# Kernel tuning notes

Measured on AMD Instinct MI355X. Metric: run time of the kernel, lower is better.

## Reference

```python
import jax, jax.numpy as jnp
import numpy as np

H = 8        # num_heads
LN_EPS = 1e-5
NEG = -1000000.0


def setup_inputs() -> dict:
    key = jax.random.key(0)
    ks = jax.random.split(key, 8)
    B, T, D = 4, 4096, 1024
    s = 1.0 / np.sqrt(D)
    x = jax.random.normal(ks[0], (B, T, D), dtype=jnp.float32)
    tmask = (jnp.arange(T) < (3 * T) // 4).astype(jnp.float32)
    src_mask = jnp.broadcast_to(tmask[None, :, None], (B, T, 1)).astype(jnp.float32)
    Wq = jax.random.normal(ks[1], (D, D), dtype=jnp.float32) * s
    Wk = jax.random.normal(ks[2], (D, D), dtype=jnp.float32) * s
    Wv = jax.random.normal(ks[3], (D, D), dtype=jnp.float32) * s
    bq = jnp.zeros((D,), jnp.float32)
    bk = jnp.zeros((D,), jnp.float32)
    bv = jnp.zeros((D,), jnp.float32)
    gamma = jnp.ones((D,), jnp.float32)
    beta = jnp.zeros((D,), jnp.float32)
    return {"x": x, "src_mask": src_mask, "Wq": Wq, "bq": bq, "Wk": Wk,
            "bk": bk, "Wv": Wv, "bv": bv, "gamma": gamma, "beta": beta}


def reference(x, src_mask, Wq, bq, Wk, bk, Wv, bv, gamma, beta):
    B, T, D = x.shape
    Dh = D // H
    # LayerNorm (same normed input feeds q, k, v)
    mu = jnp.mean(x, axis=-1, keepdims=True)
    var = jnp.mean(jnp.square(x - mu), axis=-1, keepdims=True)
    xn = (x - mu) * jax.lax.rsqrt(var + LN_EPS) * gamma + beta
    q = xn @ Wq + bq                               # [B,T,D]
    k = xn @ Wk + bk + (1.0 - src_mask) * NEG      # mask padded timesteps
    v = (xn @ Wv + bv) * src_mask                  # zero padded values
    q = jax.nn.softmax(q.reshape(B, T, H, Dh), axis=-1)   # over feature dim
    k = jax.nn.softmax(k.reshape(B, T, H, Dh), axis=1)    # over time dim
    v = v.reshape(B, T, H, Dh)
    # efficient/linear attention: O(T * Dh^2) per head
    att = jnp.einsum('bnhd,bnhl->bhdl', k, v)      # [B,H,Dh,Dh]
    y = jnp.einsum('bnhd,bhdl->bnhl', q, att).reshape(B, T, D)
    return x + y
```

## Files before the change

### kernel.cpp

```cpp
#include <hip/hip_runtime.h>
#include <stdint.h>


typedef unsigned short u16;
typedef __attribute__((ext_vector_type(8))) short bf16x8;
typedef __attribute__((ext_vector_type(4))) float f32x4;

__device__ u16 g_WT[3][1024 * 1024];
__device__ u16 g_xn[16777216];
__device__ u16 g_ekT[16777216];
__device__ u16 g_vvT[16777216];
__device__ float g_attp[8388608];
__device__ u16 g_attT[524288];
__device__ float g_Z[4096];

__device__ __forceinline__ float b2f(u16 u) {
  union { unsigned int i; float f; } c;
  c.i = ((unsigned int)u) << 16;
  return c.f;
}
__device__ __forceinline__ u16 f2b(float f) {
  union { float f; unsigned int i; } c;
  c.f = f;
  unsigned int r = c.i + 0x7fffu + ((c.i >> 16) & 1u);
  return (u16)(r >> 16);
}

__device__ __forceinline__ void gload16(const void* g, void* l) {
  __builtin_amdgcn_global_load_lds(
      reinterpret_cast<const __attribute__((address_space(1))) uint32_t*>(
          reinterpret_cast<uintptr_t>(g)),
      reinterpret_cast<__attribute__((address_space(3))) uint32_t*>(
          reinterpret_cast<uintptr_t>(l)),
      16, 0, 0);
}

__device__ __forceinline__ void stage128x32(const u16* g, int stride, char* lds,
                                            int wave, int lane) {
  const int r = wave * 32 + (lane >> 2);
  const int cb = (lane & 3) * 16;
  const char* gp = (const char*)g;
  gload16(gp + (size_t)r * stride * 2 + cb, lds + wave * 2048);
  gload16(gp + (size_t)(r + 16) * stride * 2 + cb, lds + wave * 2048 + 1024);
}

__device__ __forceinline__ bf16x8 frag_ld(const char* lds, int row, int lane) {
  return *(const bf16x8*)(lds + row * 64 + ((lane >> 4) * 16));
}

__device__ __forceinline__ void tile_mfma(const char* As, const char* Bs,
                                          f32x4 (&acc)[4][4], int wm, int wn,
                                          int lane) {
  bf16x8 af[4], bfr[4];
#pragma unroll
  for (int i = 0; i < 4; i++) af[i] = frag_ld(As, wm * 64 + i * 16 + (lane & 15), lane);
#pragma unroll
  for (int j = 0; j < 4; j++) bfr[j] = frag_ld(Bs, wn * 64 + j * 16 + (lane & 15), lane);
#pragma unroll
  for (int i = 0; i < 4; i++)
#pragma unroll
    for (int j = 0; j < 4; j++)
      acc[i][j] = __builtin_amdgcn_mfma_f32_16x16x32_bf16(af[i], bfr[j], acc[i][j], 0, 0, 0);
}

__device__ __forceinline__ void stageA256(char* buf, const u16* gsrc, int h,
                                          int wave, int lane) {
#pragma unroll
  for (int i = 0; i < 2; i++) {
    const int ib = i * 64 + wave * 8;
    const int rowb = (ib & 63) | ((ib & 64) << 1) | (h << 6);
    const int row = rowb + (lane >> 3);
    const int cc = (lane & 7) ^ (row & 7);
    gload16((const char*)gsrc + ((size_t)row * 1024 + cc * 8) * 2,
            buf + rowb * 128);
  }
}
__device__ __forceinline__ void stageB256(char* buf, const u16* gsrc, int h,
                                          int wave, int lane) {
#pragma unroll
  for (int i = 0; i < 2; i++) {
    const int ib = i * 64 + wave * 8;
    const int rowb = (ib & 31) | ((ib & 96) << 1) | (h << 5);
    const int row = rowb + (lane >> 3);
    const int cc = (lane & 7) ^ (row & 7);
    gload16((const char*)gsrc + ((size_t)row * 1024 + cc * 8) * 2,
            buf + rowb * 128);
  }
}
__device__ __forceinline__ bf16x8 fragS(const char* buf, int R, int ks, int lane) {
  const int q = lane >> 4;
  return *(const bf16x8*)(buf + R * 128 + ((((ks << 2) + q) ^ (R & 7)) << 4));
}

__global__ __launch_bounds__(256) void prep_kernel(const float* __restrict__ x,
                                                   const float* __restrict__ gamma,
                                                   const float* __restrict__ beta,
                                                   const float* __restrict__ wq,
                                                   const float* __restrict__ wk,
                                                   const float* __restrict__ wv) {
  __shared__ float ls[4], ls2[4];
  __shared__ u16 tile[32][33];
  const int bid = blockIdx.x;
  const int tid = threadIdx.x;
  if (bid < 16384) {
    if (bid < 16) g_Z[bid * 256 + tid] = 0.0f;
    const int wave = tid >> 6, lane = tid & 63;
    const float* xr = x + (size_t)bid * 1024;
    float4 u = ((const float4*)xr)[tid];
    float v0 = u.x, v1 = u.y, v2 = u.z, v3 = u.w;
    float s = v0 + v1 + v2 + v3;
    float s2 = v0 * v0 + v1 * v1 + v2 * v2 + v3 * v3;
#pragma unroll
    for (int off = 32; off > 0; off >>= 1) {
      s += __shfl_down(s, off);
      s2 += __shfl_down(s2, off);
    }
    if (lane == 0) { ls[wave] = s; ls2[wave] = s2; }
    __syncthreads();
    s = ls[0] + ls[1] + ls[2] + ls[3];
    s2 = ls2[0] + ls2[1] + ls2[2] + ls2[3];
    const float mu = s * (1.0f / 1024.0f);
    const float var = fmaxf(s2 * (1.0f / 1024.0f) - mu * mu, 0.0f);
    const float rstd = rsqrtf(var + 1e-5f);
    float4 g4 = ((const float4*)gamma)[tid];
    float4 be = ((const float4*)beta)[tid];
    ushort4 o;
    o.x = f2b((v0 - mu) * rstd * g4.x + be.x);
    o.y = f2b((v1 - mu) * rstd * g4.y + be.y);
    o.z = f2b((v2 - mu) * rstd * g4.z + be.z);
    o.w = f2b((v3 - mu) * rstd * g4.w + be.w);
    *(ushort4*)(g_xn + (size_t)bid * 1024 + tid * 4) = o;
  } else {
    const int id = bid - 16384;
    const int which = id >> 10;
    const int rem = id & 1023;
    const float* src = (which == 0) ? wq : (which == 1) ? wk : wv;
    u16* dst = g_WT[which];
    const int tx = tid & 31;
    const int ty = tid >> 5;
    const int c0 = (rem & 31) * 32, r0 = (rem >> 5) * 32;
#pragma unroll
    for (int i = 0; i < 4; i++)
      tile[ty + i * 8][tx] = f2b(src[(size_t)(r0 + ty + i * 8) * 1024 + c0 + tx]);
    __syncthreads();
#pragma unroll
    for (int i = 0; i < 4; i++)
      dst[(size_t)(c0 + ty + i * 8) * 1024 + r0 + tx] = tile[tx][ty + i * 8];
  }
}

__global__ __launch_bounds__(512, 2) void gemm_kv(const float* __restrict__ bk,
                                                  const float* __restrict__ bv,
                                                  const float* __restrict__ mask) {
  __shared__ __align__(16) char smem[131072];
  const int tid = threadIdx.x, wave = tid >> 6, lane = tid & 63;
  const int L = blockIdx.x;
  const int mt = (L & 7) + 8 * (L >> 6);
  const int nt = (L >> 3) & 7;
  const int n0 = (nt & 3) * 256;
  const int z = nt >> 2;
  const int m0 = mt * 256;
  const u16* wt = z ? g_WT[2] : g_WT[1];
  const float* bias = z ? bv : bk;
  u16* outT = z ? g_vvT : g_ekT;
  const int b = m0 >> 12;
  const int t0 = m0 & 4095;
  const int wm = wave >> 2, wn = wave & 3;
  const u16* Ag = g_xn + (size_t)m0 * 1024;
  const u16* Bg = wt + (size_t)n0 * 1024;

  f32x4 zero = {0.f, 0.f, 0.f, 0.f};
  f32x4 acc[8][4];
#pragma unroll
  for (int i = 0; i < 8; i++)
#pragma unroll
    for (int j = 0; j < 4; j++) acc[i][j] = zero;
  bf16x8 a[4][2], bB[2][2][2];

  stageA256(smem, Ag, 0, wave, lane);
  stageB256(smem + 65536, Bg, 0, wave, lane);
  stageA256(smem, Ag, 1, wave, lane);
  stageB256(smem + 65536, Bg, 1, wave, lane);
  asm volatile("s_waitcnt vmcnt(0)" ::: "memory");
  __builtin_amdgcn_s_barrier();

#pragma unroll 1
  for (int t = 0; t < 16; ++t) {
    const int p = t & 1;
    char* Ab = smem + p * 32768;
    char* Bb = smem + 65536 + p * 32768;
    char* An = smem + (p ^ 1) * 32768;
    char* Bn = smem + 65536 + (p ^ 1) * 32768;
    const u16* Agn = Ag + (t + 1) * 64;
    const u16* Bgn = Bg + (t + 1) * 64;
    const bool st = t < 15;

#pragma unroll
    for (int rf = 0; rf < 4; rf++) {
      const int R = wm * 128 + rf * 16 + (lane & 15);
#pragma unroll
      for (int ks = 0; ks < 2; ks++) a[rf][ks] = fragS(Ab, R, ks, lane);
    }
#pragma unroll
    for (int cf = 0; cf < 2; cf++) {
      const int R = wn * 64 + cf * 16 + (lane & 15);
#pragma unroll
      for (int ks = 0; ks < 2; ks++) bB[0][cf][ks] = fragS(Bb, R, ks, lane);
    }
    if (st) {
      stageA256(An, Agn, 0, wave, lane);
      stageB256(Bn, Bgn, 0, wave, lane);
      asm volatile("s_waitcnt vmcnt(4)" ::: "memory");
    } else {
      asm volatile("s_waitcnt vmcnt(0)" ::: "memory");
    }
    __builtin_amdgcn_s_barrier();
    asm volatile("s_waitcnt lgkmcnt(0)" ::: "memory");
    __builtin_amdgcn_sched_barrier(0);
    __builtin_amdgcn_s_setprio(1);
#pragma unroll
    for (int rf = 0; rf < 4; rf++)
#pragma unroll
      for (int cf = 0; cf < 2; cf++)
#pragma unroll
        for (int ks = 0; ks < 2; ks++)
          acc[rf][cf] = __builtin_amdgcn_mfma_f32_16x16x32_bf16(
              a[rf][ks], bB[0][cf][ks], acc[rf][cf], 0, 0, 0);
    __builtin_amdgcn_s_setprio(0);
    __builtin_amdgcn_s_barrier();
    __builtin_amdgcn_sched_barrier(0);

#pragma unroll
    for (int cf = 0; cf < 2; cf++) {
      const int R = wn * 64 + 32 + cf * 16 + (lane & 15);
#pragma unroll
      for (int ks = 0; ks < 2; ks++) bB[1][cf][ks] = fragS(Bb, R, ks, lane);
    }
    if (st) stageB256(Bn, Bgn, 1, wave, lane);
    __builtin_amdgcn_s_barrier();
    asm volatile("s_waitcnt lgkmcnt(0)" ::: "memory");
    __builtin_amdgcn_sched_barrier(0);
    __builtin_amdgcn_s_setprio(1);
#pragma unroll
    for (int rf = 0; rf < 4; rf++)
#pragma unroll
      for (int cf = 0; cf < 2; cf++)
#pragma unroll
        for (int ks = 0; ks < 2; ks++)
          acc[rf][2 + cf] = __builtin_amdgcn_mfma_f32_16x16x32_bf16(
              a[rf][ks], bB[1][cf][ks], acc[rf][2 + cf], 0, 0, 0);
    __builtin_amdgcn_s_setprio(0);
    __builtin_amdgcn_s_barrier();
    __builtin_amdgcn_sched_barrier(0);

#pragma unroll
    for (int rf = 0; rf < 4; rf++) {
      const int R = wm * 128 + 64 + rf * 16 + (lane & 15);
#pragma unroll
      for (int ks = 0; ks < 2; ks++) a[rf][ks] = fragS(Ab, R, ks, lane);
    }
    if (st) stageA256(An, Agn, 1, wave, lane);
    asm volatile("s_waitcnt vmcnt(4)" ::: "memory");
    __builtin_amdgcn_s_barrier();
    asm volatile("s_waitcnt lgkmcnt(0)" ::: "memory");
    __builtin_amdgcn_sched_barrier(0);
    __builtin_amdgcn_s_setprio(1);
#pragma unroll
    for (int rf = 0; rf < 4; rf++)
#pragma unroll
      for (int cf = 0; cf < 2; cf++)
#pragma unroll
        for (int ks = 0; ks < 2; ks++)
          acc[4 + rf][2 + cf] = __builtin_amdgcn_mfma_f32_16x16x32_bf16(
              a[rf][ks], bB[1][cf][ks], acc[4 + rf][2 + cf], 0, 0, 0);
    __builtin_amdgcn_s_setprio(0);
    __builtin_amdgcn_s_barrier();
    __builtin_amdgcn_sched_barrier(0);

    asm volatile("s_waitcnt vmcnt(2)" ::: "memory");
    __builtin_amdgcn_s_barrier();
    __builtin_amdgcn_s_setprio(1);
#pragma unroll
    for (int rf = 0; rf < 4; rf++)
#pragma unroll
      for (int cf = 0; cf < 2; cf++)
#pragma unroll
        for (int ks = 0; ks < 2; ks++)
          acc[4 + rf][cf] = __builtin_amdgcn_mfma_f32_16x16x32_bf16(
              a[rf][ks], bB[0][cf][ks], acc[4 + rf][cf], 0, 0, 0);
    __builtin_amdgcn_s_setprio(0);
    __builtin_amdgcn_s_barrier();
    __builtin_amdgcn_sched_barrier(0);
  }

  u16* tT = (u16*)smem;
  float fsum[4] = {0.f, 0.f, 0.f, 0.f};
#pragma unroll
  for (int rf = 0; rf < 8; rf++)
#pragma unroll
    for (int r = 0; r < 4; r++) {
      const int tok = wm * 128 + rf * 16 + (lane >> 4) * 4 + r;
      const float mv = mask[m0 + tok];
#pragma unroll
      for (int cf = 0; cf < 4; cf++) {
        const int feat = wn * 64 + cf * 16 + (lane & 15);
        const float aV = acc[rf][cf][r] + bias[n0 + feat];
        float o;
        if (z)
          o = aV * mv;
        else
          o = (mv > 0.5f) ? __expf(fminf(aV, 30.0f)) : 0.0f;
        const u16 ob = f2b(o);
        tT[feat * 256 + ((((tok >> 3) ^ (feat & 7)) << 3) | (tok & 7))] = ob;
        if (!z) fsum[cf] += b2f(ob);
      }
    }
  if (!z) {
#pragma unroll
    for (int cf = 0; cf < 4; cf++) {
      float s = fsum[cf];
      s += __shfl_xor(s, 16);
      s += __shfl_xor(s, 32);
      if (lane < 16)
        atomicAdd(&g_Z[b * 1024 + n0 + wn * 64 + cf * 16 + lane], s);
    }
  }
  __syncthreads();
  const size_t gbase = (size_t)b * (1024 * 4096) + (size_t)n0 * 4096 + t0;
#pragma unroll
  for (int u = 0; u < 16; u++) {
    const int id = u * 512 + tid;
    const int feat = id >> 5, c = id & 31;
    uint4 val = *(const uint4*)&tT[feat * 256 + ((c ^ (feat & 7)) << 3)];
    *(uint4*)(outT + gbase + (size_t)feat * 4096 + c * 8) = val;
  }
}

__global__ __launch_bounds__(256) void gemm_att() {
  __shared__ __align__(16) char smem[32768];
  char* A0 = smem;
  char* B0 = smem + 8192;
  char* A1 = smem + 16384;
  char* B1 = smem + 24576;
  const int tid = threadIdx.x, wave = tid >> 6, lane = tid & 63;
  const int kc = blockIdx.x;
  const int bh = blockIdx.y;
  const int b = bh >> 3, h = bh & 7;
  const size_t base = (size_t)b * (1024 * 4096) + (size_t)(h * 128) * 4096;
  const int wm = wave & 1, wn = wave >> 1;
  const u16* Ag = g_ekT + base + kc * 256;
  const u16* Bg = g_vvT + base + kc * 256;

  f32x4 zero = {0.f, 0.f, 0.f, 0.f};
  f32x4 acc[4][4];
#pragma unroll
  for (int i = 0; i < 4; i++)
#pragma unroll
    for (int j = 0; j < 4; j++) acc[i][j] = zero;

  stage128x32(Ag, 4096, A0, wave, lane);
  stage128x32(Bg, 4096, B0, wave, lane);
  __syncthreads();
  for (int kt = 0; kt < 256; kt += 64) {
    stage128x32(Ag + kt + 32, 4096, A1, wave, lane);
    stage128x32(Bg + kt + 32, 4096, B1, wave, lane);
    tile_mfma(A0, B0, acc, wm, wn, lane);
    __syncthreads();
    if (kt + 64 < 256) {
      stage128x32(Ag + kt + 64, 4096, A0, wave, lane);
      stage128x32(Bg + kt + 64, 4096, B0, wave, lane);
    }
    tile_mfma(A1, B1, acc, wm, wn, lane);
    __syncthreads();
  }

  float* op = g_attp + ((size_t)(kc * 32 + bh)) * 16384;
#pragma unroll
  for (int i = 0; i < 4; i++)
#pragma unroll
    for (int r = 0; r < 4; r++) {
      const int row = wm * 64 + i * 16 + (lane >> 4) * 4 + r;
#pragma unroll
      for (int j = 0; j < 4; j++) {
        const int col = wn * 64 + j * 16 + (lane & 15);
        op[row * 128 + col] = acc[i][j][r];
      }
    }
}

__global__ __launch_bounds__(256) void attnorm_kernel() {
  const int bh = blockIdx.x;
  const int b = bh >> 3, h = bh & 7;
  const int tid = threadIdx.x;
  __shared__ float Zl[128];
  if (tid < 128) Zl[tid] = fmaxf(g_Z[b * 1024 + h * 128 + tid], 1e-30f);
  __syncthreads();
  const int i0 = blockIdx.y * 2048;
  for (int i = i0 + tid; i < i0 + 2048; i += 256) {
    const int d = i >> 7, l = i & 127;
    float s = 0.f;
#pragma unroll
    for (int c = 0; c < 16; c++) s += g_attp[((size_t)(c * 32 + bh)) * 16384 + i];
    g_attT[(size_t)bh * 16384 + l * 128 + d] = f2b(s / Zl[d]);
  }
}

__global__ __launch_bounds__(256) void gemm_qy(const float* __restrict__ bq,
                                               const float* __restrict__ x,
                                               float* __restrict__ out) {
  __shared__ __align__(16) char smem[51200];
  __shared__ float zqp[2][128];
  char* A0 = smem;
  char* B0 = smem + 8192;
  char* A1 = smem + 16384;
  char* B1 = smem + 24576;
  u16* qs = (u16*)smem;
  char* C0 = smem + 34816;
  char* C1 = smem + 43008;
  const int tid = threadIdx.x, wave = tid >> 6, lane = tid & 63;
  const int L = blockIdx.x;
  const int c = L & 7;
  const int k = L >> 3;
  const int h = k & 7;
  const int m0 = (c + 8 * (k >> 3)) * 128;
  const int b = m0 >> 12;
  const int bh = b * 8 + h;
  const int wm = wave & 1, wn = wave >> 1;
  const u16* Ag = g_xn + (size_t)m0 * 1024;
  const u16* Bg = g_WT[0] + (size_t)(h * 128) * 1024;
  const u16* Cg = g_attT + (size_t)bh * 16384;

  f32x4 zero = {0.f, 0.f, 0.f, 0.f};
  f32x4 acc[4][4];
#pragma unroll
  for (int i = 0; i < 4; i++)
#pragma unroll
    for (int j = 0; j < 4; j++) acc[i][j] = zero;

  stage128x32(Ag, 1024, A0, wave, lane);
  stage128x32(Bg, 1024, B0, wave, lane);
  __syncthreads();
  for (int k0 = 0; k0 < 1024; k0 += 64) {
    stage128x32(Ag + k0 + 32, 1024, A1, wave, lane);
    stage128x32(Bg + k0 + 32, 1024, B1, wave, lane);
    tile_mfma(A0, B0, acc, wm, wn, lane);
    __syncthreads();
    if (k0 + 64 < 1024) {
      stage128x32(Ag + k0 + 64, 1024, A0, wave, lane);
      stage128x32(Bg + k0 + 64, 1024, B0, wave, lane);
    }
    tile_mfma(A1, B1, acc, wm, wn, lane);
    __syncthreads();
  }

  stage128x32(Cg, 128, C0, wave, lane);

#pragma unroll
  for (int i = 0; i < 4; i++)
#pragma unroll
    for (int r = 0; r < 4; r++) {
      const int rowl = wm * 64 + i * 16 + (lane >> 4) * 4 + r;
      float rs = 0.f;
#pragma unroll
      for (int j = 0; j < 4; j++) {
        const int coll = wn * 64 + j * 16 + (lane & 15);
        const float e = __expf(fminf(acc[i][j][r] + bq[h * 128 + coll], 30.0f));
        qs[rowl * 136 + coll] = f2b(e);
        rs += e;
      }
      rs += __shfl_xor(rs, 1);
      rs += __shfl_xor(rs, 2);
      rs += __shfl_xor(rs, 4);
      rs += __shfl_xor(rs, 8);
      if ((lane & 15) == 0) zqp[wn][rowl] = rs;
    }
  __syncthreads();

  f32x4 acc2[4][4];
#pragma unroll
  for (int i = 0; i < 4; i++)
#pragma unroll
    for (int j = 0; j < 4; j++) acc2[i][j] = zero;

  for (int k0 = 0; k0 < 128; k0 += 64) {
    stage128x32(Cg + k0 + 32, 128, C1, wave, lane);
    {
      bf16x8 af[4], bfr[4];
#pragma unroll
      for (int i = 0; i < 4; i++)
        af[i] = *(const bf16x8*)&qs[(wm * 64 + i * 16 + (lane & 15)) * 136 + k0 + (lane >> 4) * 8];
#pragma unroll
      for (int j = 0; j < 4; j++) bfr[j] = frag_ld(C0, wn * 64 + j * 16 + (lane & 15), lane);
#pragma unroll
      for (int i = 0; i < 4; i++)
#pragma unroll
        for (int j = 0; j < 4; j++)
          acc2[i][j] = __builtin_amdgcn_mfma_f32_16x16x32_bf16(af[i], bfr[j], acc2[i][j], 0, 0, 0);
    }
    __syncthreads();
    if (k0 + 64 < 128) stage128x32(Cg + k0 + 64, 128, C0, wave, lane);
    {
      bf16x8 af[4], bfr[4];
#pragma unroll
      for (int i = 0; i < 4; i++)
        af[i] = *(const bf16x8*)&qs[(wm * 64 + i * 16 + (lane & 15)) * 136 + k0 + 32 + (lane >> 4) * 8];
#pragma unroll
      for (int j = 0; j < 4; j++) bfr[j] = frag_ld(C1, wn * 64 + j * 16 + (lane & 15), lane);
#pragma unroll
      for (int i = 0; i < 4; i++)
#pragma unroll
        for (int j = 0; j < 4; j++)
          acc2[i][j] = __builtin_amdgcn_mfma_f32_16x16x32_bf16(af[i], bfr[j], acc2[i][j], 0, 0, 0);
    }
    __syncthreads();
  }

#pragma unroll
  for (int i = 0; i < 4; i++)
#pragma unroll
    for (int r = 0; r < 4; r++) {
      const int rowl = wm * 64 + i * 16 + (lane >> 4) * 4 + r;
      const float zq = fmaxf(zqp[0][rowl] + zqp[1][rowl], 1e-30f);
      const size_t n = (size_t)m0 + rowl;
#pragma unroll
      for (int j = 0; j < 4; j++) {
        const int coll = wn * 64 + j * 16 + (lane & 15);
        const size_t idx = n * 1024 + h * 128 + coll;
        out[idx] = x[idx] + acc2[i][j][r] / zq;
      }
    }
}

extern "C" void kernel_launch(void* const* d_in, const int* in_sizes, int n_in,
                              void* d_out, int out_size, void* d_ws, size_t ws_size,
                              hipStream_t stream) {
  const float* x = (const float*)d_in[0];
  const float* mask = (const float*)d_in[1];
  const float* Wq = (const float*)d_in[2];
  const float* bq = (const float*)d_in[3];
  const float* Wk = (const float*)d_in[4];
  const float* bk = (const float*)d_in[5];
  const float* Wv = (const float*)d_in[6];
  const float* bv = (const float*)d_in[7];
  const float* gamma = (const float*)d_in[8];
  const float* beta = (const float*)d_in[9];
  float* out = (float*)d_out;
  (void)d_ws; (void)ws_size;

  prep_kernel<<<dim3(16384 + 3072), 256, 0, stream>>>(x, gamma, beta, Wq, Wk, Wv);
  gemm_kv<<<dim3(512), 512, 0, stream>>>(bk, bv, mask);
  gemm_att<<<dim3(16, 32), 256, 0, stream>>>();
  attnorm_kernel<<<dim3(32, 8), 256, 0, stream>>>();
  gemm_qy<<<dim3(1024), 256, 0, stream>>>(bq, x, out);
}
```

Baseline: 335.4 us.

## Restructure K/V projection GEMM main loop to prefetch two K-tiles ahead

The K/V projection GEMM loop now keeps two K-tiles in flight instead of one. Each LDS buffer is refilled in place with the tile two steps ahead, right after its fragments are read into registers. The loop body is factored into a templated four-phase helper with compile-time wait counts, and the loop is unrolled by two over the buffers. This aims to hide more global-load latency behind MFMA work, at the cost of tighter ordering between barriers and in-place overwrites of LDS.

```diff
diff --git a/kernel.cpp b/kernel.cpp
--- a/kernel.cpp
+++ b/kernel.cpp
@@ -90,6 +90,110 @@
 __device__ __forceinline__ bf16x8 fragS(const char* buf, int R, int ks, int lane) {
   const int q = lane >> 4;
   return *(const bf16x8*)(buf + R * 128 + ((((ks << 2) + q) ^ (R & 7)) << 4));
+}
+
+template<int WAIT, bool ST>
+__device__ __forceinline__ void kv_4ph(char* Ab, char* Bb, const u16* Agn,
+                                       const u16* Bgn, f32x4 (&acc)[8][4],
+                                       int wave, int lane, int wm, int wn) {
+  bf16x8 a[4][2], b0[2][2], b1[2][2];
+
+#pragma unroll
+  for (int rf = 0; rf < 4; rf++) {
+    const int R = wm * 128 + rf * 16 + (lane & 15);
+#pragma unroll
+    for (int ks = 0; ks < 2; ks++) a[rf][ks] = fragS(Ab, R, ks, lane);
+  }
+#pragma unroll
+  for (int cf = 0; cf < 2; cf++) {
+    const int R = wn * 64 + cf * 16 + (lane & 15);
+#pragma unroll
+    for (int ks = 0; ks < 2; ks++) b0[cf][ks] = fragS(Bb, R, ks, lane);
+  }
+  __builtin_amdgcn_s_barrier();
+  asm volatile("s_waitcnt lgkmcnt(0)" ::: "memory");
+  __builtin_amdgcn_sched_barrier(0);
+  __builtin_amdgcn_s_setprio(1);
+#pragma unroll
+  for (int rf = 0; rf < 4; rf++)
+#pragma unroll
+    for (int cf = 0; cf < 2; cf++)
+#pragma unroll
+      for (int ks = 0; ks < 2; ks++)
+        acc[rf][cf] = __builtin_amdgcn_mfma_f32_16x16x32_bf16(
+            a[rf][ks], b0[cf][ks], acc[rf][cf], 0, 0, 0);
+  __builtin_amdgcn_s_setprio(0);
+  __builtin_amdgcn_s_barrier();
+  __builtin_amdgcn_sched_barrier(0);
+
+#pragma unroll
+  for (int cf = 0; cf < 2; cf++) {
+    const int R = wn * 64 + 32 + cf * 16 + (lane & 15);
+#pragma unroll
+    for (int ks = 0; ks < 2; ks++) b1[cf][ks] = fragS(Bb, R, ks, lane);
+  }
+  if constexpr (ST) {
+    stageA256(Ab, Agn, 0, wave, lane);
+    stageB256(Bb, Bgn, 0, wave, lane);
+  }
+  __builtin_amdgcn_s_barrier();
+  asm volatile("s_waitcnt lgkmcnt(0)" ::: "memory");
+  __builtin_amdgcn_sched_barrier(0);
+  __builtin_amdgcn_s_setprio(1);
+#pragma unroll
+  for (int rf = 0; rf < 4; rf++)
+#pragma unroll
+    for (int cf = 0; cf < 2; cf++)
+#pragma unroll
+      for (int ks = 0; ks < 2; ks++)
+        acc[rf][2 + cf] = __builtin_amdgcn_mfma_f32_16x16x32_bf16(
+            a[rf][ks], b1[cf][ks], acc[rf][2 + cf], 0, 0, 0);
+  __builtin_amdgcn_s_setprio(0);
+  __builtin_amdgcn_s_barrier();
+  __builtin_amdgcn_sched_barrier(0);
+
+#pragma unroll
+  for (int rf = 0; rf < 4; rf++) {
+    const int R = wm * 128 + 64 + rf * 16 + (lane & 15);
+#pragma unroll
+    for (int ks = 0; ks < 2; ks++) a[rf][ks] = fragS(Ab, R, ks, lane);
+  }
+  if constexpr (ST) stageB256(Bb, Bgn, 1, wave, lane);
+  __builtin_amdgcn_s_barrier();
+  asm volatile("s_waitcnt lgkmcnt(0)" ::: "memory");
+  __builtin_amdgcn_sched_barrier(0);
+  __builtin_amdgcn_s_setprio(1);
+#pragma unroll
+  for (int rf = 0; rf < 4; rf++)
+#pragma unroll
+    for (int cf = 0; cf < 2; cf++)
+#pragma unroll
+      for (int ks = 0; ks < 2; ks++)
+        acc[4 + rf][2 + cf] = __builtin_amdgcn_mfma_f32_16x16x32_bf16(
+            a[rf][ks], b1[cf][ks], acc[4 + rf][2 + cf], 0, 0, 0);
+  __builtin_amdgcn_s_setprio(0);
+  __builtin_amdgcn_s_barrier();
+  __builtin_amdgcn_sched_barrier(0);
+
+  if constexpr (ST) stageA256(Ab, Agn, 1, wave, lane);
+  if constexpr (WAIT == 8) {
+    asm volatile("s_waitcnt vmcnt(8)" ::: "memory");
+  } else if constexpr (WAIT == 0) {
+    asm volatile("s_waitcnt vmcnt(0)" ::: "memory");
+  }
+  __builtin_amdgcn_s_barrier();
+  __builtin_amdgcn_s_setprio(1);
+#pragma unroll
+  for (int rf = 0; rf < 4; rf++)
+#pragma unroll
+    for (int cf = 0; cf < 2; cf++)
+#pragma unroll
+      for (int ks = 0; ks < 2; ks++)
+        acc[4 + rf][cf] = __builtin_amdgcn_mfma_f32_16x16x32_bf16(
+            a[rf][ks], b0[cf][ks], acc[4 + rf][cf], 0, 0, 0);
+  __builtin_amdgcn_s_setprio(0);
+  __builtin_amdgcn_s_barrier();
+  __builtin_amdgcn_sched_barrier(0);
 }
 
 __global__ __launch_bounds__(256) void prep_kernel(const float* __restrict__ x,
@@ -169,129 +273,38 @@
   const u16* Ag = g_xn + (size_t)m0 * 1024;
   const u16* Bg = wt + (size_t)n0 * 1024;
 
+  char* A0 = smem;
+  char* A1 = smem + 32768;
+  char* B0 = smem + 65536;
+  char* B1 = smem + 98304;
+
   f32x4 zero = {0.f, 0.f, 0.f, 0.f};
   f32x4 acc[8][4];
 #pragma unroll
   for (int i = 0; i < 8; i++)
 #pragma unroll
     for (int j = 0; j < 4; j++) acc[i][j] = zero;
-  bf16x8 a[4][2], bB[2][2][2];
-
-  stageA256(smem, Ag, 0, wave, lane);
-  stageB256(smem + 65536, Bg, 0, wave, lane);
-  stageA256(smem, Ag, 1, wave, lane);
-  stageB256(smem + 65536, Bg, 1, wave, lane);
-  asm volatile("s_waitcnt vmcnt(0)" ::: "memory");
+
+  stageA256(A0, Ag, 0, wave, lane);
+  stageA256(A0, Ag, 1, wave, lane);
+  stageB256(B0, Bg, 0, wave, lane);
+  stageB256(B0, Bg, 1, wave, lane);
+  stageA256(A1, Ag + 64, 0, wave, lane);
+  stageA256(A1, Ag + 64, 1, wave, lane);
+  stageB256(B1, Bg + 64, 0, wave, lane);
+  stageB256(B1, Bg + 64, 1, wave, lane);
+  asm volatile("s_waitcnt vmcnt(8)" ::: "memory");
   __builtin_amdgcn_s_barrier();
 
 #pragma unroll 1
-  for (int t = 0; t < 16; ++t) {
-    const int p = t & 1;
-    char* Ab = smem + p * 32768;
-    char* Bb = smem + 65536 + p * 32768;
-    char* An = smem + (p ^ 1) * 32768;
-    char* Bn = smem + 65536 + (p ^ 1) * 32768;
-    const u16* Agn = Ag + (t + 1) * 64;
-    const u16* Bgn = Bg + (t + 1) * 64;
-    const bool st = t < 15;
-
-#pragma unroll
-    for (int rf = 0; rf < 4; rf++) {
-      const int R = wm * 128 + rf * 16 + (lane & 15);
-#pragma unroll
-      for (int ks = 0; ks < 2; ks++) a[rf][ks] = fragS(Ab, R, ks, lane);
-    }
-#pragma unroll
-    for (int cf = 0; cf < 2; cf++) {
-      const int R = wn * 64 + cf * 16 + (lane & 15);
-#pragma unroll
-      for (int ks = 0; ks < 2; ks++) bB[0][cf][ks] = fragS(Bb, R, ks, lane);
-    }
-    if (st) {
-      stageA256(An, Agn, 0, wave, lane);
-      stageB256(Bn, Bgn, 0, wave, lane);
-      asm volatile("s_waitcnt vmcnt(4)" ::: "memory");
-    } else {
-      asm volatile("s_waitcnt vmcnt(0)" ::: "memory");
-    }
-    __builtin_amdgcn_s_barrier();
-    asm volatile("s_waitcnt lgkmcnt(0)" ::: "memory");
-    __builtin_amdgcn_sched_barrier(0);
-    __builtin_amdgcn_s_setprio(1);
-#pragma unroll
-    for (int rf = 0; rf < 4; rf++)
-#pragma unroll
-      for (int cf = 0; cf < 2; cf++)
-#pragma unroll
-        for (int ks = 0; ks < 2; ks++)
-          acc[rf][cf] = __builtin_amdgcn_mfma_f32_16x16x32_bf16(
-              a[rf][ks], bB[0][cf][ks], acc[rf][cf], 0, 0, 0);
-    __builtin_amdgcn_s_setprio(0);
-    __builtin_amdgcn_s_barrier();
-    __builtin_amdgcn_sched_barrier(0);
-
-#pragma unroll
-    for (int cf = 0; cf < 2; cf++) {
-      const int R = wn * 64 + 32 + cf * 16 + (lane & 15);
-#pragma unroll
-      for (int ks = 0; ks < 2; ks++) bB[1][cf][ks] = fragS(Bb, R, ks, lane);
-    }
-    if (st) stageB256(Bn, Bgn, 1, wave, lane);
-    __builtin_amdgcn_s_barrier();
-    asm volatile("s_waitcnt lgkmcnt(0)" ::: "memory");
-    __builtin_amdgcn_sched_barrier(0);
-    __builtin_amdgcn_s_setprio(1);
-#pragma unroll
-    for (int rf = 0; rf < 4; rf++)
-#pragma unroll
-      for (int cf = 0; cf < 2; cf++)
-#pragma unroll
-        for (int ks = 0; ks < 2; ks++)
-          acc[rf][2 + cf] = __builtin_amdgcn_mfma_f32_16x16x32_bf16(
-              a[rf][ks], bB[1][cf][ks], acc[rf][2 + cf], 0, 0, 0);
-    __builtin_amdgcn_s_setprio(0);
-    __builtin_amdgcn_s_barrier();
-    __builtin_amdgcn_sched_barrier(0);
-
-#pragma unroll
-    for (int rf = 0; rf < 4; rf++) {
-      const int R = wm * 128 + 64 + rf * 16 + (lane & 15);
-#pragma unroll
-      for (int ks = 0; ks < 2; ks++) a[rf][ks] = fragS(Ab, R, ks, lane);
-    }
-    if (st) stageA256(An, Agn, 1, wave, lane);
-    asm volatile("s_waitcnt vmcnt(4)" ::: "memory");
-    __builtin_amdgcn_s_barrier();
-    asm volatile("s_waitcnt lgkmcnt(0)" ::: "memory");
-    __builtin_amdgcn_sched_barrier(0);
-    __builtin_amdgcn_s_setprio(1);
-#pragma unroll
-    for (int rf = 0; rf < 4; rf++)
-#pragma unroll
-      for (int cf = 0; cf < 2; cf++)
-#pragma unroll
-        for (int ks = 0; ks < 2; ks++)
-          acc[4 + rf][2 + cf] = __builtin_amdgcn_mfma_f32_16x16x32_bf16(
-              a[rf][ks], bB[1][cf][ks], acc[4 + rf][2 + cf], 0, 0, 0);
-    __builtin_amdgcn_s_setprio(0);
-    __builtin_amdgcn_s_barrier();
-    __builtin_amdgcn_sched_barrier(0);
-
-    asm volatile("s_waitcnt vmcnt(2)" ::: "memory");
-    __builtin_amdgcn_s_barrier();
-    __builtin_amdgcn_s_setprio(1);
-#pragma unroll
-    for (int rf = 0; rf < 4; rf++)
-#pragma unroll
-      for (int cf = 0; cf < 2; cf++)
-#pragma unroll
-        for (int ks = 0; ks < 2; ks++)
-          acc[4 + rf][cf] = __builtin_amdgcn_mfma_f32_16x16x32_bf16(
-              a[rf][ks], bB[0][cf][ks], acc[4 + rf][cf], 0, 0, 0);
-    __builtin_amdgcn_s_setprio(0);
-    __builtin_amdgcn_s_barrier();
-    __builtin_amdgcn_sched_barrier(0);
-  }
+  for (int t = 0; t < 14; t += 2) {
+    kv_4ph<8, true>(A0, B0, Ag + (t + 2) * 64, Bg + (t + 2) * 64, acc, wave,
+                    lane, wm, wn);
+    kv_4ph<8, true>(A1, B1, Ag + (t + 3) * 64, Bg + (t + 3) * 64, acc, wave,
+                    lane, wm, wn);
+  }
+  kv_4ph<0, false>(A0, B0, Ag, Bg, acc, wave, lane, wm, wn);
+  kv_4ph<-1, false>(A1, B1, Ag, Bg, acc, wave, lane, wm, wn);
 
   u16* tT = (u16*)smem;
   float fsum[4] = {0.f, 0.f, 0.f, 0.f};
```

Measured after the change: 336.8 us. No clear change (+0.4%).

## Rewrite Q GEMM to reuse the 256x256 pipelined tile from the KV GEMM

Applied to the files above, without the earlier changes.

Pulls the pipelined 256x256 MFMA tile body out of gemm_kv into a shared templated helper, peeling the last iteration. gemm_qy now uses that tile with 512 threads, 128KB of LDS and a swizzled layout for the exp(q) tile. Each block covers two heads and reads the attention matrix directly from global memory. The goal is more data reuse per block and a better-overlapped main GEMM. In exchange the grid drops to 256 blocks, and the large LDS footprint may limit occupancy.

```diff
diff --git a/kernel.cpp b/kernel.cpp
--- a/kernel.cpp
+++ b/kernel.cpp
@@ -90,6 +90,111 @@
 __device__ __forceinline__ bf16x8 fragS(const char* buf, int R, int ks, int lane) {
   const int q = lane >> 4;
   return *(const bf16x8*)(buf + R * 128 + ((((ks << 2) + q) ^ (R & 7)) << 4));
+}
+
+template <bool ST>
+__device__ __forceinline__ void tile_r8(char* Ab, char* Bb, char* An, char* Bn,
+                                        const u16* Agn, const u16* Bgn,
+                                        f32x4 (&acc)[8][4], int wave, int lane,
+                                        int wm, int wn) {
+  bf16x8 a[4][2], bB[2][2][2];
+
+#pragma unroll
+  for (int rf = 0; rf < 4; rf++) {
+    const int R = wm * 128 + rf * 16 + (lane & 15);
+#pragma unroll
+    for (int ks = 0; ks < 2; ks++) a[rf][ks] = fragS(Ab, R, ks, lane);
+  }
+#pragma unroll
+  for (int cf = 0; cf < 2; cf++) {
+    const int R = wn * 64 + cf * 16 + (lane & 15);
+#pragma unroll
+    for (int ks = 0; ks < 2; ks++) bB[0][cf][ks] = fragS(Bb, R, ks, lane);
+  }
+  if constexpr (ST) {
+    stageA256(An, Agn, 0, wave, lane);
+    stageB256(Bn, Bgn, 0, wave, lane);
+    asm volatile("s_waitcnt vmcnt(4)" ::: "memory");
+  } else {
+    asm volatile("s_waitcnt vmcnt(0)" ::: "memory");
+  }
+  __builtin_amdgcn_s_barrier();
+  asm volatile("s_waitcnt lgkmcnt(0)" ::: "memory");
+  __builtin_amdgcn_sched_barrier(0);
+  __builtin_amdgcn_s_setprio(1);
+#pragma unroll
+  for (int rf = 0; rf < 4; rf++)
+#pragma unroll
+    for (int cf = 0; cf < 2; cf++)
+#pragma unroll
+      for (int ks = 0; ks < 2; ks++)
+        acc[rf][cf] = __builtin_amdgcn_mfma_f32_16x16x32_bf16(
+            a[rf][ks], bB[0][cf][ks], acc[rf][cf], 0, 0, 0);
+  __builtin_amdgcn_s_setprio(0);
+  __builtin_amdgcn_s_barrier();
+  __builtin_amdgcn_sched_barrier(0);
+
+#pragma unroll
+  for (int cf = 0; cf < 2; cf++) {
+    const int R = wn * 64 + 32 + cf * 16 + (lane & 15);
+#pragma unroll
+    for (int ks = 0; ks < 2; ks++) bB[1][cf][ks] = fragS(Bb, R, ks, lane);
+  }
+  if constexpr (ST) stageB256(Bn, Bgn, 1, wave, lane);
+  __builtin_amdgcn_s_barrier();
+  asm volatile("s_waitcnt lgkmcnt(0)" ::: "memory");
+  __builtin_amdgcn_sched_barrier(0);
+  __builtin_amdgcn_s_setprio(1);
+#pragma unroll
+  for (int rf = 0; rf < 4; rf++)
+#pragma unroll
+    for (int cf = 0; cf < 2; cf++)
+#pragma unroll
+      for (int ks = 0; ks < 2; ks++)
+        acc[rf][2 + cf] = __builtin_amdgcn_mfma_f32_16x16x32_bf16(
+            a[rf][ks], bB[1][cf][ks], acc[rf][2 + cf], 0, 0, 0);
+  __builtin_amdgcn_s_setprio(0);
+  __builtin_amdgcn_s_barrier();
+  __builtin_amdgcn_sched_barrier(0);
+
+#pragma unroll
+  for (int rf = 0; rf < 4; rf++) {
+    const int R = wm * 128 + 64 + rf * 16 + (lane & 15);
+#pragma unroll
+    for (int ks = 0; ks < 2; ks++) a[rf][ks] = fragS(Ab, R, ks, lane);
+  }
+  if constexpr (ST) stageA256(An, Agn, 1, wave, lane);
+  asm volatile("s_waitcnt vmcnt(4)" ::: "memory");
+  __builtin_amdgcn_s_barrier();
+  asm volatile("s_waitcnt lgkmcnt(0)" ::: "memory");
+  __builtin_amdgcn_sched_barrier(0);
+  __builtin_amdgcn_s_setprio(1);
+#pragma unroll
+  for (int rf = 0; rf < 4; rf++)
+#pragma unroll
+    for (int cf = 0; cf < 2; cf++)
+#pragma unroll
+      for (int ks = 0; ks < 2; ks++)
+        acc[4 + rf][2 + cf] = __builtin_amdgcn_mfma_f32_16x16x32_bf16(
+            a[rf][ks], bB[1][cf][ks], acc[4 + rf][2 + cf], 0, 0, 0);
+  __builtin_amdgcn_s_setprio(0);
+  __builtin_amdgcn_s_barrier();
+  __builtin_amdgcn_sched_barrier(0);
+
+  asm volatile("s_waitcnt vmcnt(2)" ::: "memory");
+  __builtin_amdgcn_s_barrier();
+  __builtin_amdgcn_s_setprio(1);
+#pragma unroll
+  for (int rf = 0; rf < 4; rf++)
+#pragma unroll
+    for (int cf = 0; cf < 2; cf++)
+#pragma unroll
+      for (int ks = 0; ks < 2; ks++)
+        acc[4 + rf][cf] = __builtin_amdgcn_mfma_f32_16x16x32_bf16(
+            a[rf][ks], bB[0][cf][ks], acc[4 + rf][cf], 0, 0, 0);
+  __builtin_amdgcn_s_setprio(0);
+  __builtin_amdgcn_s_barrier();
+  __builtin_amdgcn_sched_barrier(0);
 }
 
 __global__ __launch_bounds__(256) void prep_kernel(const float* __restrict__ x,
@@ -175,7 +280,6 @@
   for (int i = 0; i < 8; i++)
 #pragma unroll
     for (int j = 0; j < 4; j++) acc[i][j] = zero;
-  bf16x8 a[4][2], bB[2][2][2];
 
   stageA256(smem, Ag, 0, wave, lane);
   stageB256(smem + 65536, Bg, 0, wave, lane);
@@ -185,113 +289,14 @@
   __builtin_amdgcn_s_barrier();
 
 #pragma unroll 1
-  for (int t = 0; t < 16; ++t) {
+  for (int t = 0; t < 15; ++t) {
     const int p = t & 1;
-    char* Ab = smem + p * 32768;
-    char* Bb = smem + 65536 + p * 32768;
-    char* An = smem + (p ^ 1) * 32768;
-    char* Bn = smem + 65536 + (p ^ 1) * 32768;
-    const u16* Agn = Ag + (t + 1) * 64;
-    const u16* Bgn = Bg + (t + 1) * 64;
-    const bool st = t < 15;
-
-#pragma unroll
-    for (int rf = 0; rf < 4; rf++) {
-      const int R = wm * 128 + rf * 16 + (lane & 15);
-#pragma unroll
-      for (int ks = 0; ks < 2; ks++) a[rf][ks] = fragS(Ab, R, ks, lane);
-    }
-#pragma unroll
-    for (int cf = 0; cf < 2; cf++) {
-      const int R = wn * 64 + cf * 16 + (lane & 15);
-#pragma unroll
-      for (int ks = 0; ks < 2; ks++) bB[0][cf][ks] = fragS(Bb, R, ks, lane);
-    }
-    if (st) {
-      stageA256(An, Agn, 0, wave, lane);
-      stageB256(Bn, Bgn, 0, wave, lane);
-      asm volatile("s_waitcnt vmcnt(4)" ::: "memory");
-    } else {
-      asm volatile("s_waitcnt vmcnt(0)" ::: "memory");
-    }
-    __builtin_amdgcn_s_barrier();
-    asm volatile("s_waitcnt lgkmcnt(0)" ::: "memory");
-    __builtin_amdgcn_sched_barrier(0);
-    __builtin_amdgcn_s_setprio(1);
-#pragma unroll
-    for (int rf = 0; rf < 4; rf++)
-#pragma unroll
-      for (int cf = 0; cf < 2; cf++)
-#pragma unroll
-        for (int ks = 0; ks < 2; ks++)
-          acc[rf][cf] = __builtin_amdgcn_mfma_f32_16x16x32_bf16(
-              a[rf][ks], bB[0][cf][ks], acc[rf][cf], 0, 0, 0);
-    __builtin_amdgcn_s_setprio(0);
-    __builtin_amdgcn_s_barrier();
-    __builtin_amdgcn_sched_barrier(0);
-
-#pragma unroll
-    for (int cf = 0; cf < 2; cf++) {
-      const int R = wn * 64 + 32 + cf * 16 + (lane & 15);
-#pragma unroll
-      for (int ks = 0; ks < 2; ks++) bB[1][cf][ks] = fragS(Bb, R, ks, lane);
-    }
-    if (st) stageB256(Bn, Bgn, 1, wave, lane);
-    __builtin_amdgcn_s_barrier();
-    asm volatile("s_waitcnt lgkmcnt(0)" ::: "memory");
-    __builtin_amdgcn_sched_barrier(0);
-    __builtin_amdgcn_s_setprio(1);
-#pragma unroll
-    for (int rf = 0; rf < 4; rf++)
-#pragma unroll
-      for (int cf = 0; cf < 2; cf++)
-#pragma unroll
-        for (int ks = 0; ks < 2; ks++)
-          acc[rf][2 + cf] = __builtin_amdgcn_mfma_f32_16x16x32_bf16(
-              a[rf][ks], bB[1][cf][ks], acc[rf][2 + cf], 0, 0, 0);
-    __builtin_amdgcn_s_setprio(0);
-    __builtin_amdgcn_s_barrier();
-    __builtin_amdgcn_sched_barrier(0);
-
-#pragma unroll
-    for (int rf = 0; rf < 4; rf++) {
-      const int R = wm * 128 + 64 + rf * 16 + (lane & 15);
-#pragma unroll
-      for (int ks = 0; ks < 2; ks++) a[rf][ks] = fragS(Ab, R, ks, lane);
-    }
-    if (st) stageA256(An, Agn, 1, wave, lane);
-    asm volatile("s_waitcnt vmcnt(4)" ::: "memory");
-    __builtin_amdgcn_s_barrier();
-    asm volatile("s_waitcnt lgkmcnt(0)" ::: "memory");
-    __builtin_amdgcn_sched_barrier(0);
-    __builtin_amdgcn_s_setprio(1);
-#pragma unroll
-    for (int rf = 0; rf < 4; rf++)
-#pragma unroll
-      for (int cf = 0; cf < 2; cf++)
-#pragma unroll
-        for (int ks = 0; ks < 2; ks++)
-          acc[4 + rf][2 + cf] = __builtin_amdgcn_mfma_f32_16x16x32_bf16(
-              a[rf][ks], bB[1][cf][ks], acc[4 + rf][2 + cf], 0, 0, 0);
-    __builtin_amdgcn_s_setprio(0);
-    __builtin_amdgcn_s_barrier();
-    __builtin_amdgcn_sched_barrier(0);
-
-    asm volatile("s_waitcnt vmcnt(2)" ::: "memory");
-    __builtin_amdgcn_s_barrier();
-    __builtin_amdgcn_s_setprio(1);
-#pragma unroll
-    for (int rf = 0; rf < 4; rf++)
-#pragma unroll
-      for (int cf = 0; cf < 2; cf++)
-#pragma unroll
-        for (int ks = 0; ks < 2; ks++)
-          acc[4 + rf][cf] = __builtin_amdgcn_mfma_f32_16x16x32_bf16(
-              a[rf][ks], bB[0][cf][ks], acc[4 + rf][cf], 0, 0, 0);
-    __builtin_amdgcn_s_setprio(0);
-    __builtin_amdgcn_s_barrier();
-    __builtin_amdgcn_sched_barrier(0);
-  }
+    tile_r8<true>(smem + p * 32768, smem + 65536 + p * 32768,
+                  smem + (p ^ 1) * 32768, smem + 65536 + (p ^ 1) * 32768,
+                  Ag + (t + 1) * 64, Bg + (t + 1) * 64, acc, wave, lane, wm, wn);
+  }
+  tile_r8<false>(smem + 32768, smem + 65536 + 32768, smem, smem + 65536, Ag, Bg,
+                 acc, wave, lane, wm, wn);
 
   u16* tT = (u16*)smem;
   float fsum[4] = {0.f, 0.f, 0.f, 0.f};
@@ -405,128 +410,113 @@
   }
 }
 
-__global__ __launch_bounds__(256) void gemm_qy(const float* __restrict__ bq,
-                                               const float* __restrict__ x,
-                                               float* __restrict__ out) {
-  __shared__ __align__(16) char smem[51200];
-  __shared__ float zqp[2][128];
-  char* A0 = smem;
-  char* B0 = smem + 8192;
-  char* A1 = smem + 16384;
-  char* B1 = smem + 24576;
-  u16* qs = (u16*)smem;
-  char* C0 = smem + 34816;
-  char* C1 = smem + 43008;
+__global__ __launch_bounds__(512, 2) void gemm_qy(const float* __restrict__ bq,
+                                                  const float* __restrict__ x,
+                                                  float* __restrict__ out) {
+  __shared__ __align__(16) char smem[131072];
+  __shared__ float zq4[4][256];
   const int tid = threadIdx.x, wave = tid >> 6, lane = tid & 63;
   const int L = blockIdx.x;
-  const int c = L & 7;
-  const int k = L >> 3;
-  const int h = k & 7;
-  const int m0 = (c + 8 * (k >> 3)) * 128;
+  const int g = L >> 3;
+  const int mt = (L & 7) + 8 * (g >> 2);
+  const int n0 = (g & 3) * 256;
+  const int m0 = mt * 256;
   const int b = m0 >> 12;
-  const int bh = b * 8 + h;
-  const int wm = wave & 1, wn = wave >> 1;
+  const int wm = wave >> 2, wn = wave & 3;
   const u16* Ag = g_xn + (size_t)m0 * 1024;
-  const u16* Bg = g_WT[0] + (size_t)(h * 128) * 1024;
-  const u16* Cg = g_attT + (size_t)bh * 16384;
+  const u16* Bg = g_WT[0] + (size_t)n0 * 1024;
 
   f32x4 zero = {0.f, 0.f, 0.f, 0.f};
-  f32x4 acc[4][4];
-#pragma unroll
-  for (int i = 0; i < 4; i++)
+  f32x4 acc[8][4];
+#pragma unroll
+  for (int i = 0; i < 8; i++)
 #pragma unroll
     for (int j = 0; j < 4; j++) acc[i][j] = zero;
 
-  stage128x32(Ag, 1024, A0, wave, lane);
-  stage128x32(Bg, 1024, B0, wave, lane);
-  __syncthreads();
-  for (int k0 = 0; k0 < 1024; k0 += 64) {
-    stage128x32(Ag + k0 + 32, 1024, A1, wave, lane);
-    stage128x32(Bg + k0 + 32, 1024, B1, wave, lane);
-    tile_mfma(A0, B0, acc, wm, wn, lane);
-    __syncthreads();
-    if (k0 + 64 < 1024) {
-      stage128x32(Ag + k0 + 64, 1024, A0, wave, lane);
-      stage128x32(Bg + k0 + 64, 1024, B0, wave, lane);
-    }
-    tile_mfma(A1, B1, acc, wm, wn, lane);
-    __syncthreads();
-  }
-
-  stage128x32(Cg, 128, C0, wave, lane);
-
-#pragma unroll
-  for (int i = 0; i < 4; i++)
+  stageA256(smem, Ag, 0, wave, lane);
+  stageB256(smem + 65536, Bg, 0, wave, lane);
+  stageA256(smem, Ag, 1, wave, lane);
+  stageB256(smem + 65536, Bg, 1, wave, lane);
+  asm volatile("s_waitcnt vmcnt(0)" ::: "memory");
+  __builtin_amdgcn_s_barrier();
+
+#pragma unroll 1
+  for (int t = 0; t < 15; ++t) {
+    const int p = t & 1;
+    tile_r8<true>(smem + p * 32768, smem + 65536 + p * 32768,
+                  smem + (p ^ 1) * 32768, smem + 65536 + (p ^ 1) * 32768,
+                  Ag + (t + 1) * 64, Bg + (t + 1) * 64, acc, wave, lane, wm, wn);
+  }
+  tile_r8<false>(smem + 32768, smem + 65536 + 32768, smem, smem + 65536, Ag, Bg,
+                 acc, wave, lane, wm, wn);
+
+  u16* qs = (u16*)smem;
+#pragma unroll
+  for (int rf = 0; rf < 8; rf++)
 #pragma unroll
     for (int r = 0; r < 4; r++) {
-      const int rowl = wm * 64 + i * 16 + (lane >> 4) * 4 + r;
+      const int tok = wm * 128 + rf * 16 + (lane >> 4) * 4 + r;
       float rs = 0.f;
 #pragma unroll
-      for (int j = 0; j < 4; j++) {
-        const int coll = wn * 64 + j * 16 + (lane & 15);
-        const float e = __expf(fminf(acc[i][j][r] + bq[h * 128 + coll], 30.0f));
-        qs[rowl * 136 + coll] = f2b(e);
+      for (int cf = 0; cf < 4; cf++) {
+        const int f = wn * 64 + cf * 16 + (lane & 15);
+        const float e = __expf(fminf(acc[rf][cf][r] + bq[n0 + f], 30.0f));
+        qs[tok * 256 + ((((f >> 3) ^ (tok & 31)) << 3) | (f & 7))] = f2b(e);
         rs += e;
       }
       rs += __shfl_xor(rs, 1);
       rs += __shfl_xor(rs, 2);
       rs += __shfl_xor(rs, 4);
       rs += __shfl_xor(rs, 8);
-      if ((lane & 15) == 0) zqp[wn][rowl] = rs;
+      if ((lane & 15) == 0) zq4[wn][tok] = rs;
     }
   __syncthreads();
 
-  f32x4 acc2[4][4];
-#pragma unroll
-  for (int i = 0; i < 4; i++)
+  const int hl = wn >> 1;
+  const int bhh = b * 8 + (n0 >> 7) + hl;
+  const u16* attb = g_attT + ((size_t)bhh << 14);
+  f32x4 acc2[8][4];
+#pragma unroll
+  for (int i = 0; i < 8; i++)
 #pragma unroll
     for (int j = 0; j < 4; j++) acc2[i][j] = zero;
 
-  for (int k0 = 0; k0 < 128; k0 += 64) {
-    stage128x32(Cg + k0 + 32, 128, C1, wave, lane);
-    {
-      bf16x8 af[4], bfr[4];
-#pragma unroll
-      for (int i = 0; i < 4; i++)
-        af[i] = *(const bf16x8*)&qs[(wm * 64 + i * 16 + (lane & 15)) * 136 + k0 + (lane >> 4) * 8];
-#pragma unroll
-      for (int j = 0; j < 4; j++) bfr[j] = frag_ld(C0, wn * 64 + j * 16 + (lane & 15), lane);
-#pragma unroll
-      for (int i = 0; i < 4; i++)
-#pragma unroll
-        for (int j = 0; j < 4; j++)
-          acc2[i][j] = __builtin_amdgcn_mfma_f32_16x16x32_bf16(af[i], bfr[j], acc2[i][j], 0, 0, 0);
-    }
-    __syncthreads();
-    if (k0 + 64 < 128) stage128x32(Cg + k0 + 64, 128, C0, wave, lane);
-    {
-      bf16x8 af[4], bfr[4];
-#pragma unroll
-      for (int i = 0; i < 4; i++)
-        af[i] = *(const bf16x8*)&qs[(wm * 64 + i * 16 + (lane & 15)) * 136 + k0 + 32 + (lane >> 4) * 8];
-#pragma unroll
-      for (int j = 0; j < 4; j++) bfr[j] = frag_ld(C1, wn * 64 + j * 16 + (lane & 15), lane);
-#pragma unroll
-      for (int i = 0; i < 4; i++)
-#pragma unroll
-        for (int j = 0; j < 4; j++)
-          acc2[i][j] = __builtin_amdgcn_mfma_f32_16x16x32_bf16(af[i], bfr[j], acc2[i][j], 0, 0, 0);
-    }
-    __syncthreads();
-  }
-
-#pragma unroll
-  for (int i = 0; i < 4; i++)
+#pragma unroll
+  for (int ks = 0; ks < 4; ks++) {
+    bf16x8 bf[4];
+#pragma unroll
+    for (int cf = 0; cf < 4; cf++) {
+      const int l = (wn & 1) * 64 + cf * 16 + (lane & 15);
+      bf[cf] = *(const bf16x8*)(attb + l * 128 + ks * 32 + (lane >> 4) * 8);
+    }
+    bf16x8 af[8];
+#pragma unroll
+    for (int rf = 0; rf < 8; rf++) {
+      const int tok = wm * 128 + rf * 16 + (lane & 15);
+      af[rf] = *(const bf16x8*)&qs[tok * 256 +
+          ((((hl << 4) + (ks << 2) + (lane >> 4)) ^ (tok & 31)) << 3)];
+    }
+#pragma unroll
+    for (int rf = 0; rf < 8; rf++)
+#pragma unroll
+      for (int cf = 0; cf < 4; cf++)
+        acc2[rf][cf] = __builtin_amdgcn_mfma_f32_16x16x32_bf16(
+            af[rf], bf[cf], acc2[rf][cf], 0, 0, 0);
+  }
+
+#pragma unroll
+  for (int rf = 0; rf < 8; rf++)
 #pragma unroll
     for (int r = 0; r < 4; r++) {
-      const int rowl = wm * 64 + i * 16 + (lane >> 4) * 4 + r;
-      const float zq = fmaxf(zqp[0][rowl] + zqp[1][rowl], 1e-30f);
-      const size_t n = (size_t)m0 + rowl;
-#pragma unroll
-      for (int j = 0; j < 4; j++) {
-        const int coll = wn * 64 + j * 16 + (lane & 15);
-        const size_t idx = n * 1024 + h * 128 + coll;
-        out[idx] = x[idx] + acc2[i][j][r] / zq;
+      const int tok = wm * 128 + rf * 16 + (lane >> 4) * 4 + r;
+      const float zq =
+          fmaxf(zq4[hl * 2][tok] + zq4[hl * 2 + 1][tok], 1e-30f);
+      const size_t n = (size_t)(m0 + tok);
+#pragma unroll
+      for (int cf = 0; cf < 4; cf++) {
+        const int f = wn * 64 + cf * 16 + (lane & 15);
+        const size_t idx = n * 1024 + n0 + f;
+        out[idx] = x[idx] + acc2[rf][cf][r] / zq;
       }
     }
 }
@@ -551,5 +541,5 @@
   gemm_kv<<<dim3(512), 512, 0, stream>>>(bk, bv, mask);
   gemm_att<<<dim3(16, 32), 256, 0, stream>>>();
   attnorm_kernel<<<dim3(32, 8), 256, 0, stream>>>();
-  gemm_qy<<<dim3(1024), 256, 0, stream>>>(bq, x, out);
-}
+  gemm_qy<<<dim3(256), 512, 0, stream>>>(bq, x, out);
+}
```

Measured after the change: 331.6 us. No clear change (-1.1%).
